# Kernel optimization log

Measured on AMD Instinct MI355X. Metric: run time of the kernel, lower is better.

## Reference

```python
import jax, jax.numpy as jnp
import numpy as np

EPS = 1e-12   # F.normalize eps
COS_EPS = 1e-8  # F.cosine_similarity eps

B, S, V, D, P, L = 4, 2048, 64, 1024, 8, 24
H = D // 24            # prefix_transform bottleneck = 42
K = 2 * L * D          # 49152 output feature dim


def setup_inputs() -> dict:
    key = jax.random.key(0)
    ks = jax.random.split(key, 8)
    return {
        "prefix": jax.random.randint(ks[0], (B, V), 0, V),
        "ctx_embeds": jax.random.normal(ks[1], (B, S, D), jnp.float32),
        "tables": jax.random.normal(ks[2], (P, V, D), jnp.float32) * 0.02,
        "lora_prefix_emb": jax.random.normal(ks[3], (P, D), jnp.float32),
        "w1": jax.random.normal(ks[4], (D, H), jnp.float32) * 0.02,
        "b1": jnp.zeros((H,), jnp.float32),
        "w2": jax.random.normal(ks[5], (H, K), jnp.float32) * 0.02,
        "b2": jnp.zeros((K,), jnp.float32),
    }


def _gates(ctx_embeds, lora_prefix_emb):
    """select_prefix, vectorized over the num_prefix_set loop.

    The original builds sim_i = bmm(norm(emb), norm(e_i.repeat(B,S,1), dim=0).permute)
    of shape [B,S,S]; since the key is repeated, every column of sim is identical,
    so we carry the column vector [P,B,S] and the math is exact.
    """
    b, s, _ = ctx_embeds.shape
    # normalize embedding over feature dim (F.normalize p=2 dim=2)
    emb_n = ctx_embeds / jnp.maximum(
        jnp.linalg.norm(ctx_embeds, axis=2, keepdims=True), EPS)
    # F.normalize over dim=0 of a tensor repeated B times -> sign(x)/sqrt(B)
    u = lora_prefix_emb / jnp.maximum(
        jnp.sqrt(float(b)) * jnp.abs(lora_prefix_emb), EPS)  # [P,D]
    v = jnp.einsum('bsd,pd->pbs', emb_n, u)          # column of sim matrix
    c = jnp.maximum(v, 0.0)                          # clamp(min=0)
    # F.normalize over last dim (length S, all entries equal c) -> c/(sqrt(S)*c)
    n = c / jnp.maximum(jnp.sqrt(float(s)) * c, EPS)
    w = jax.nn.softmax(n, axis=2)                    # softmax over token dim (dim=1 in torch layout)
    a_v = jnp.einsum('pbs,bsd->pbd', w, ctx_embeds)  # attended value per expert
    e_norm = jnp.linalg.norm(lora_prefix_emb, axis=1)          # [P]
    a_norm = jnp.linalg.norm(a_v, axis=2)                      # [P,B]
    cos = jnp.einsum('pd,pbd->pb', lora_prefix_emb, a_v) / \
        jnp.maximum(e_norm[:, None] * a_norm, COS_EPS)
    return jax.nn.softmax(cos.T, axis=-1)            # self.s_t, [B,P]


def reference(prefix, ctx_embeds, tables, lora_prefix_emb, w1, b1, w2, b2):
    s_t = _gates(ctx_embeds, lora_prefix_emb)        # [B,P]
    # forward() re-applies softmax to self.s_t (faithful double softmax)
    gate = jax.nn.softmax(s_t, axis=-1)              # [B,P]
    tok = tables[:, prefix]                          # [P,B,V,D] per-expert embedding lookup
    h = jnp.tanh(jnp.einsum('pbvd,dh->pbvh', tok, w1) + b1)
    pkv = jnp.einsum('pbvh,hk->pbvk', h, w2) + b2    # [P,B,V,K]
    out = jnp.einsum('bp,pbvk->bvk', gate, pkv)      # gated mixture over experts
    return out
```

## Files before the change

kernel.cpp:

```cpp
#include <hip/hip_runtime.h>

#define BB 4
#define SS 2048
#define VV 64
#define DD 1024
#define PP 8
#define HH 42
#define KK 49152

static constexpr float F_EPS = 1e-12f;
static constexpr float ALPHA = 1.02234304f;

__global__ __launch_bounds__(512) void kU_fused(
    const float* __restrict__ ctx, const float* __restrict__ lora,
    const float* __restrict__ tables, const float* __restrict__ w1,
    const float* __restrict__ b1, float* __restrict__ part,
    float* __restrict__ h_all) {
  __shared__ float smem[PP * DD + 16 + 32 * PP];
  const int t = threadIdx.x;
  const int b = blockIdx.y;
  if (blockIdx.x < 64) {
    const int chunk = blockIdx.x;
    float* u_lds = smem;
    float* w_lds = smem + PP * DD + 16;
    for (int i = t; i < PP * DD; i += 512) {
      float e = lora[i];
      u_lds[i] = e / fmaxf(2.0f * fabsf(e), F_EPS);
    }
    __syncthreads();
    const int wave = t >> 6, lane = t & 63;
    const int rbase = b * SS + chunk * 32 + wave * 4;
    const float4* ctx4 = (const float4*)ctx;
    const float4* u4 = (const float4*)u_lds;
    float dot[4][PP];
    #pragma unroll
    for (int i = 0; i < 4; ++i)
      #pragma unroll
      for (int p = 0; p < PP; ++p) dot[i][p] = 0.f;
    #pragma unroll
    for (int j = 0; j < 4; ++j) {
      float4 c[4];
      #pragma unroll
      for (int i = 0; i < 4; ++i)
        c[i] = ctx4[(size_t)(rbase + i) * 256 + j * 64 + lane];
      #pragma unroll
      for (int p = 0; p < PP; ++p) {
        float4 u = u4[p * 256 + j * 64 + lane];
        #pragma unroll
        for (int i = 0; i < 4; ++i)
          dot[i][p] += c[i].x * u.x + c[i].y * u.y + c[i].z * u.z + c[i].w * u.w;
      }
    }
    const int sel = lane & 7;
    #pragma unroll
    for (int i = 0; i < 4; ++i) {
      float d0 = dot[i][0], d1 = dot[i][1], d2 = dot[i][2], d3 = dot[i][3];
      float d4 = dot[i][4], d5 = dot[i][5], d6 = dot[i][6], d7 = dot[i][7];
      #pragma unroll
      for (int m = 1; m <= 4; m <<= 1) {
        d0 += __shfl_xor(d0, m, 64); d1 += __shfl_xor(d1, m, 64);
        d2 += __shfl_xor(d2, m, 64); d3 += __shfl_xor(d3, m, 64);
        d4 += __shfl_xor(d4, m, 64); d5 += __shfl_xor(d5, m, 64);
        d6 += __shfl_xor(d6, m, 64); d7 += __shfl_xor(d7, m, 64);
      }
      float v = d0;
      v = (sel == 1) ? d1 : v; v = (sel == 2) ? d2 : v;
      v = (sel == 3) ? d3 : v; v = (sel == 4) ? d4 : v;
      v = (sel == 5) ? d5 : v; v = (sel == 6) ? d6 : v;
      v = (sel == 7) ? d7 : v;
      v += __shfl_xor(v, 8, 64);
      v += __shfl_xor(v, 16, 64);
      v += __shfl_xor(v, 32, 64);
      if (lane < PP)
        w_lds[(wave * 4 + i) * PP + lane] = (v > 0.0f) ? ALPHA : 1.0f;
    }
    __syncthreads();
    float2 acc[PP];
    #pragma unroll
    for (int p = 0; p < PP; ++p) acc[p] = make_float2(0.f, 0.f);
    const float2* ctx2 = (const float2*)ctx;
    const float4* w4 = (const float4*)w_lds;
    #pragma unroll 4
    for (int sl = 0; sl < 32; ++sl) {
      float2 c = ctx2[(size_t)(b * SS + chunk * 32 + sl) * 512 + t];
      float4 wa = w4[sl * 2];
      float4 wb = w4[sl * 2 + 1];
      float w[PP] = {wa.x, wa.y, wa.z, wa.w, wb.x, wb.y, wb.z, wb.w};
      #pragma unroll
      for (int p = 0; p < PP; ++p) {
        acc[p].x += w[p] * c.x;
        acc[p].y += w[p] * c.y;
      }
    }
    float2* part2 = (float2*)part;
    #pragma unroll
    for (int p = 0; p < PP; ++p)
      part2[(size_t)((b * 64 + chunk) * PP + p) * 512 + t] = acc[p];
  } else {
    float* row_lds = smem;
    float* partial = smem + DD;
    const int r = (blockIdx.x - 64) * 4 + b;
    ((float2*)row_lds)[t] = ((const float2*)(tables + (size_t)r * DD))[t];
    __syncthreads();
    const int h = t & 63, q = t >> 6;
    float acc = 0.0f;
    if (h < HH) {
      const int d0 = q * 128;
      #pragma unroll 8
      for (int dl = 0; dl < 128; ++dl) {
        acc += row_lds[d0 + dl] * w1[(size_t)(d0 + dl) * HH + h];
      }
    }
    partial[q * 64 + h] = acc;
    __syncthreads();
    if (t < HH) {
      float s = 0.0f;
      #pragma unroll
      for (int q8 = 0; q8 < 8; ++q8) s += partial[q8 * 64 + t];
      h_all[(size_t)r * HH + t] = tanhf(s + b1[t]);
    }
  }
}

__global__ __launch_bounds__(256) void k4_cos(
    const float* __restrict__ part, const float* __restrict__ lora,
    float* __restrict__ cos_ws) {
  const int t = threadIdx.x;
  const int p = blockIdx.x, b = blockIdx.y;
  const float4* part4 = (const float4*)part;
  float4 av = make_float4(0.f, 0.f, 0.f, 0.f);
  #pragma unroll 8
  for (int c = 0; c < 64; ++c) {
    float4 x = part4[(size_t)((b * 64 + c) * PP + p) * 256 + t];
    av.x += x.x; av.y += x.y; av.z += x.z; av.w += x.w;
  }
  float4 e = ((const float4*)lora)[p * 256 + t];
  float dt = av.x * e.x + av.y * e.y + av.z * e.z + av.w * e.w;
  float a2 = av.x * av.x + av.y * av.y + av.z * av.z + av.w * av.w;
  float e2 = e.x * e.x + e.y * e.y + e.z * e.z + e.w * e.w;
  #pragma unroll
  for (int m = 32; m >= 1; m >>= 1) {
    dt += __shfl_xor(dt, m, 64);
    a2 += __shfl_xor(a2, m, 64);
    e2 += __shfl_xor(e2, m, 64);
  }
  __shared__ float red[4][3];
  const int wave = t >> 6, lane = t & 63;
  if (lane == 0) { red[wave][0] = dt; red[wave][1] = a2; red[wave][2] = e2; }
  __syncthreads();
  if (t == 0) {
    float Dv = red[0][0] + red[1][0] + red[2][0] + red[3][0];
    float Av = red[0][1] + red[1][1] + red[2][1] + red[3][1];
    float Ev = red[0][2] + red[1][2] + red[2][2] + red[3][2];
    cos_ws[b * PP + p] = Dv / fmaxf(sqrtf(Ev) * sqrtf(Av), 1e-8f);
  }
}

__global__ __launch_bounds__(256) void k7_out(
    const float* __restrict__ w2, const float* __restrict__ b2,
    const float* __restrict__ h_all, const float* __restrict__ cos_ws,
    const int* __restrict__ prefix, float* __restrict__ out) {
  __shared__ float gate_lds[PP];
  __shared__ float hg_lds[HH * 64];
  __shared__ float w2_lds[HH * 128];
  const int t = threadIdx.x;
  const int b = blockIdx.y;
  const size_t kbase = (size_t)blockIdx.x * 128;
  for (int i = t; i < HH * 128; i += 256) {
    int h = i >> 7, kk = i & 127;
    w2_lds[i] = w2[(size_t)h * KK + kbase + kk];
  }
  if (t == 0) {
    float c[PP];
    float m = -1e30f;
    #pragma unroll
    for (int p = 0; p < PP; ++p) { c[p] = cos_ws[b * PP + p]; m = fmaxf(m, c[p]); }
    float s = 0.0f;
    #pragma unroll
    for (int p = 0; p < PP; ++p) { c[p] = expf(c[p] - m); s += c[p]; }
    float inv = 1.0f / s;
    float m2 = -1e30f;
    #pragma unroll
    for (int p = 0; p < PP; ++p) { c[p] *= inv; m2 = fmaxf(m2, c[p]); }
    float s2 = 0.0f;
    #pragma unroll
    for (int p = 0; p < PP; ++p) { c[p] = expf(c[p] - m2); s2 += c[p]; }
    float inv2 = 1.0f / s2;
    #pragma unroll
    for (int p = 0; p < PP; ++p) gate_lds[p] = c[p] * inv2;
  }
  __syncthreads();
  for (int idx = t; idx < 64 * HH; idx += 256) {
    int v = idx / HH;
    int h = idx - v * HH;
    int tokv = prefix[b * VV + v];
    float s = 0.0f;
    #pragma unroll
    for (int p = 0; p < PP; ++p)
      s += gate_lds[p] * h_all[(size_t)(p * VV + tokv) * HH + h];
    hg_lds[h * 64 + v] = s;
  }
  __syncthreads();
  const int tk = t & 31, tb = t >> 5;
  float4 acc[8];
  #pragma unroll
  for (int i = 0; i < 8; ++i) acc[i] = make_float4(0.f, 0.f, 0.f, 0.f);
  const float4* w24 = (const float4*)w2_lds;
  const float4* hg4 = (const float4*)hg_lds;
  #pragma unroll 2
  for (int h = 0; h < HH; ++h) {
    float4 wv = w24[h * 32 + tk];
    float4 g0 = hg4[h * 16 + tb * 2];
    float4 g1 = hg4[h * 16 + tb * 2 + 1];
    float gg[8] = {g0.x, g0.y, g0.z, g0.w, g1.x, g1.y, g1.z, g1.w};
    #pragma unroll
    for (int i = 0; i < 8; ++i) {
      acc[i].x += gg[i] * wv.x;
      acc[i].y += gg[i] * wv.y;
      acc[i].z += gg[i] * wv.z;
      acc[i].w += gg[i] * wv.w;
    }
  }
  float4 b2v = ((const float4*)b2)[(kbase >> 2) + tk];
  float4* out4 = (float4*)out;
  #pragma unroll
  for (int i = 0; i < 8; ++i) {
    int bv = b * 64 + tb * 8 + i;
    float4 o;
    o.x = acc[i].x + b2v.x;
    o.y = acc[i].y + b2v.y;
    o.z = acc[i].z + b2v.z;
    o.w = acc[i].w + b2v.w;
    out4[(((size_t)bv * KK + kbase) >> 2) + tk] = o;
  }
}

extern "C" void kernel_launch(void* const* d_in, const int* in_sizes, int n_in,
                              void* d_out, int out_size, void* d_ws, size_t ws_size,
                              hipStream_t stream) {
  const int* prefix = (const int*)d_in[0];
  const float* ctx = (const float*)d_in[1];
  const float* tables = (const float*)d_in[2];
  const float* lora = (const float*)d_in[3];
  const float* w1 = (const float*)d_in[4];
  const float* b1 = (const float*)d_in[5];
  const float* w2 = (const float*)d_in[6];
  const float* b2 = (const float*)d_in[7];
  float* out = (float*)d_out;
  char* ws = (char*)d_ws;
  float* part = (float*)ws;
  float* cos_ws = (float*)(ws + 8388608);
  float* h_all = (float*)(ws + 8388608 + 128);

  kU_fused<<<dim3(192, 4), 512, 0, stream>>>(ctx, lora, tables, w1, b1, part, h_all);
  k4_cos<<<dim3(8, 4), 256, 0, stream>>>(part, lora, cos_ws);
  k7_out<<<dim3(384, 4), 256, 0, stream>>>(w2, b2, h_all, cos_ws, prefix, out);
}
```

Before: 151.6 us.

## Hoist gate softmax and gated hidden mix out of output kernel into dedicated pass

Splits the cosine reduction into 128 smaller single-wave blocks that emit partial dot and norm sums. A new per-batch kernel computes the double-softmax gate and the gated hidden mix once and writes it to workspace. Previously every one of the 1536 output blocks recomputed that softmax and gathered h_all itself. The output kernel now loads the precomputed mix and writes with nontemporal stores, and the ctx accumulation loop is unrolled further. The cost is one extra kernel launch and a serialized dependency.

```diff
diff --git a/kernel.cpp b/kernel.cpp
--- a/kernel.cpp
+++ b/kernel.cpp
@@ -10,6 +10,8 @@
 
 static constexpr float F_EPS = 1e-12f;
 static constexpr float ALPHA = 1.02234304f;
+
+typedef float f32x4 __attribute__((ext_vector_type(4)));
 
 __global__ __launch_bounds__(512) void kU_fused(
     const float* __restrict__ ctx, const float* __restrict__ lora,
@@ -80,7 +82,7 @@
     for (int p = 0; p < PP; ++p) acc[p] = make_float2(0.f, 0.f);
     const float2* ctx2 = (const float2*)ctx;
     const float4* w4 = (const float4*)w_lds;
-    #pragma unroll 4
+    #pragma unroll 8
     for (int sl = 0; sl < 32; ++sl) {
       float2 c = ctx2[(size_t)(b * SS + chunk * 32 + sl) * 512 + t];
       float4 wa = w4[sl * 2];
@@ -122,19 +124,19 @@
   }
 }
 
-__global__ __launch_bounds__(256) void k4_cos(
+__global__ __launch_bounds__(64) void k4_part(
     const float* __restrict__ part, const float* __restrict__ lora,
-    float* __restrict__ cos_ws) {
-  const int t = threadIdx.x;
-  const int p = blockIdx.x, b = blockIdx.y;
+    float* __restrict__ trip) {
+  const int t = threadIdx.x;
+  const int p = blockIdx.x, b = blockIdx.y, z = blockIdx.z;
   const float4* part4 = (const float4*)part;
   float4 av = make_float4(0.f, 0.f, 0.f, 0.f);
   #pragma unroll 8
   for (int c = 0; c < 64; ++c) {
-    float4 x = part4[(size_t)((b * 64 + c) * PP + p) * 256 + t];
+    float4 x = part4[(size_t)((b * 64 + c) * PP + p) * 256 + z * 64 + t];
     av.x += x.x; av.y += x.y; av.z += x.z; av.w += x.w;
   }
-  float4 e = ((const float4*)lora)[p * 256 + t];
+  float4 e = ((const float4*)lora)[p * 256 + z * 64 + t];
   float dt = av.x * e.x + av.y * e.y + av.z * e.z + av.w * e.w;
   float a2 = av.x * av.x + av.y * av.y + av.z * av.z + av.w * av.w;
   float e2 = e.x * e.x + e.y * e.y + e.z * e.z + e.w * e.w;
@@ -144,23 +146,61 @@
     a2 += __shfl_xor(a2, m, 64);
     e2 += __shfl_xor(e2, m, 64);
   }
-  __shared__ float red[4][3];
-  const int wave = t >> 6, lane = t & 63;
-  if (lane == 0) { red[wave][0] = dt; red[wave][1] = a2; red[wave][2] = e2; }
+  if (t == 0)
+    ((float4*)trip)[(b * PP + p) * 4 + z] = make_float4(dt, a2, e2, 0.f);
+}
+
+__global__ __launch_bounds__(256) void k6_gate_hg(
+    const float* __restrict__ trip, const float* __restrict__ h_all,
+    const int* __restrict__ prefix, float* __restrict__ hg) {
+  __shared__ float gate_lds[PP];
+  const int t = threadIdx.x;
+  const int b = blockIdx.x;
+  if (t < PP) {
+    const float4* tp = (const float4*)trip + ((size_t)b * PP + t) * 4;
+    float dt = 0.f, a2 = 0.f, e2 = 0.f;
+    #pragma unroll
+    for (int z = 0; z < 4; ++z) {
+      float4 x = tp[z];
+      dt += x.x; a2 += x.y; e2 += x.z;
+    }
+    gate_lds[t] = dt / fmaxf(sqrtf(e2) * sqrtf(a2), 1e-8f);
+  }
   __syncthreads();
   if (t == 0) {
-    float Dv = red[0][0] + red[1][0] + red[2][0] + red[3][0];
-    float Av = red[0][1] + red[1][1] + red[2][1] + red[3][1];
-    float Ev = red[0][2] + red[1][2] + red[2][2] + red[3][2];
-    cos_ws[b * PP + p] = Dv / fmaxf(sqrtf(Ev) * sqrtf(Av), 1e-8f);
+    float c[PP];
+    float m = -1e30f;
+    #pragma unroll
+    for (int p = 0; p < PP; ++p) { c[p] = gate_lds[p]; m = fmaxf(m, c[p]); }
+    float s = 0.0f;
+    #pragma unroll
+    for (int p = 0; p < PP; ++p) { c[p] = expf(c[p] - m); s += c[p]; }
+    float inv = 1.0f / s;
+    float m2 = -1e30f;
+    #pragma unroll
+    for (int p = 0; p < PP; ++p) { c[p] *= inv; m2 = fmaxf(m2, c[p]); }
+    float s2 = 0.0f;
+    #pragma unroll
+    for (int p = 0; p < PP; ++p) { c[p] = expf(c[p] - m2); s2 += c[p]; }
+    float inv2 = 1.0f / s2;
+    #pragma unroll
+    for (int p = 0; p < PP; ++p) gate_lds[p] = c[p] * inv2;
+  }
+  __syncthreads();
+  for (int idx = t; idx < VV * HH; idx += 256) {
+    int h = idx >> 6, v = idx & 63;
+    int tokv = prefix[b * VV + v];
+    float s = 0.0f;
+    #pragma unroll
+    for (int p = 0; p < PP; ++p)
+      s += gate_lds[p] * h_all[(size_t)(p * VV + tokv) * HH + h];
+    hg[(size_t)b * (VV * HH) + idx] = s;
   }
 }
 
 __global__ __launch_bounds__(256) void k7_out(
     const float* __restrict__ w2, const float* __restrict__ b2,
-    const float* __restrict__ h_all, const float* __restrict__ cos_ws,
-    const int* __restrict__ prefix, float* __restrict__ out) {
-  __shared__ float gate_lds[PP];
+    const float* __restrict__ hg, float* __restrict__ out) {
   __shared__ float hg_lds[HH * 64];
   __shared__ float w2_lds[HH * 128];
   const int t = threadIdx.x;
@@ -170,35 +210,8 @@
     int h = i >> 7, kk = i & 127;
     w2_lds[i] = w2[(size_t)h * KK + kbase + kk];
   }
-  if (t == 0) {
-    float c[PP];
-    float m = -1e30f;
-    #pragma unroll
-    for (int p = 0; p < PP; ++p) { c[p] = cos_ws[b * PP + p]; m = fmaxf(m, c[p]); }
-    float s = 0.0f;
-    #pragma unroll
-    for (int p = 0; p < PP; ++p) { c[p] = expf(c[p] - m); s += c[p]; }
-    float inv = 1.0f / s;
-    float m2 = -1e30f;
-    #pragma unroll
-    for (int p = 0; p < PP; ++p) { c[p] *= inv; m2 = fmaxf(m2, c[p]); }
-    float s2 = 0.0f;
-    #pragma unroll
-    for (int p = 0; p < PP; ++p) { c[p] = expf(c[p] - m2); s2 += c[p]; }
-    float inv2 = 1.0f / s2;
-    #pragma unroll
-    for (int p = 0; p < PP; ++p) gate_lds[p] = c[p] * inv2;
-  }
-  __syncthreads();
-  for (int idx = t; idx < 64 * HH; idx += 256) {
-    int v = idx / HH;
-    int h = idx - v * HH;
-    int tokv = prefix[b * VV + v];
-    float s = 0.0f;
-    #pragma unroll
-    for (int p = 0; p < PP; ++p)
-      s += gate_lds[p] * h_all[(size_t)(p * VV + tokv) * HH + h];
-    hg_lds[h * 64 + v] = s;
+  for (int i = t; i < HH * 64; i += 256) {
+    hg_lds[i] = hg[(size_t)b * (HH * 64) + i];
   }
   __syncthreads();
   const int tk = t & 31, tb = t >> 5;
@@ -222,16 +235,16 @@
     }
   }
   float4 b2v = ((const float4*)b2)[(kbase >> 2) + tk];
-  float4* out4 = (float4*)out;
+  f32x4* out4 = (f32x4*)out;
   #pragma unroll
   for (int i = 0; i < 8; ++i) {
     int bv = b * 64 + tb * 8 + i;
-    float4 o;
+    f32x4 o;
     o.x = acc[i].x + b2v.x;
     o.y = acc[i].y + b2v.y;
     o.z = acc[i].z + b2v.z;
     o.w = acc[i].w + b2v.w;
-    out4[(((size_t)bv * KK + kbase) >> 2) + tk] = o;
+    __builtin_nontemporal_store(o, out4 + (((size_t)bv * KK + kbase) >> 2) + tk);
   }
 }
 
@@ -249,10 +262,12 @@
   float* out = (float*)d_out;
   char* ws = (char*)d_ws;
   float* part = (float*)ws;
-  float* cos_ws = (float*)(ws + 8388608);
-  float* h_all = (float*)(ws + 8388608 + 128);
+  float* trip = (float*)(ws + 8388608);
+  float* hg = (float*)(ws + 8388608 + 2048);
+  float* h_all = (float*)(ws + 8388608 + 2048 + 43008);
 
   kU_fused<<<dim3(192, 4), 512, 0, stream>>>(ctx, lora, tables, w1, b1, part, h_all);
-  k4_cos<<<dim3(8, 4), 256, 0, stream>>>(part, lora, cos_ws);
-  k7_out<<<dim3(384, 4), 256, 0, stream>>>(w2, b2, h_all, cos_ws, prefix, out);
-}
+  k4_part<<<dim3(8, 4, 4), 64, 0, stream>>>(part, lora, trip);
+  k6_gate_hg<<<dim3(4, 1), 256, 0, stream>>>(trip, h_all, prefix, hg);
+  k7_out<<<dim3(384, 4), 256, 0, stream>>>(w2, b2, hg, out);
+}
```

Result: slower. 160.7 us (+6.1%).

## Fold cosine/gate reduction into first kernel via last-block atomic counter

Applied to the files above, without the earlier changes.

Each gating block now handles 128 rows instead of 32, so there are 16 chunks per batch instead of 64 and fewer partial sums. An atomic counter per batch lets the last finishing chunk block reduce the partials, compute the cosine scores and the double softmax, and write the final gates. This removes the separate k4_cos launch and the per-block softmax in k7_out, at the cost of an extra memset and less parallelism in the gating phase, now 64 blocks instead of 256.

```diff
diff --git a/kernel.cpp b/kernel.cpp
--- a/kernel.cpp
+++ b/kernel.cpp
@@ -7,19 +7,23 @@
 #define PP 8
 #define HH 42
 #define KK 49152
+#define NCHUNK 16
+#define ROWS 128
 
 static constexpr float F_EPS = 1e-12f;
 static constexpr float ALPHA = 1.02234304f;
 
-__global__ __launch_bounds__(512) void kU_fused(
+__global__ __launch_bounds__(512) void kU2(
     const float* __restrict__ ctx, const float* __restrict__ lora,
     const float* __restrict__ tables, const float* __restrict__ w1,
     const float* __restrict__ b1, float* __restrict__ part,
-    float* __restrict__ h_all) {
-  __shared__ float smem[PP * DD + 16 + 32 * PP];
+    float* __restrict__ h_all, float* __restrict__ gate_ws,
+    int* __restrict__ ctr) {
+  __shared__ float smem[PP * DD + 16 + ROWS * PP];
+  __shared__ int flag_s;
   const int t = threadIdx.x;
   const int b = blockIdx.y;
-  if (blockIdx.x < 64) {
+  if (blockIdx.x < NCHUNK) {
     const int chunk = blockIdx.x;
     float* u_lds = smem;
     float* w_lds = smem + PP * DD + 16;
@@ -29,50 +33,53 @@
     }
     __syncthreads();
     const int wave = t >> 6, lane = t & 63;
-    const int rbase = b * SS + chunk * 32 + wave * 4;
     const float4* ctx4 = (const float4*)ctx;
     const float4* u4 = (const float4*)u_lds;
-    float dot[4][PP];
-    #pragma unroll
-    for (int i = 0; i < 4; ++i)
-      #pragma unroll
-      for (int p = 0; p < PP; ++p) dot[i][p] = 0.f;
-    #pragma unroll
-    for (int j = 0; j < 4; ++j) {
-      float4 c[4];
+    const int sel = lane & 7;
+    for (int g = 0; g < 4; ++g) {
+      const int rloc = wave * 16 + g * 4;
+      const int rbase = b * SS + chunk * ROWS + rloc;
+      float dot[4][PP];
       #pragma unroll
       for (int i = 0; i < 4; ++i)
-        c[i] = ctx4[(size_t)(rbase + i) * 256 + j * 64 + lane];
-      #pragma unroll
-      for (int p = 0; p < PP; ++p) {
-        float4 u = u4[p * 256 + j * 64 + lane];
+        #pragma unroll
+        for (int p = 0; p < PP; ++p) dot[i][p] = 0.f;
+      #pragma unroll
+      for (int j = 0; j < 4; ++j) {
+        float4 c[4];
         #pragma unroll
         for (int i = 0; i < 4; ++i)
-          dot[i][p] += c[i].x * u.x + c[i].y * u.y + c[i].z * u.z + c[i].w * u.w;
-      }
-    }
-    const int sel = lane & 7;
-    #pragma unroll
-    for (int i = 0; i < 4; ++i) {
-      float d0 = dot[i][0], d1 = dot[i][1], d2 = dot[i][2], d3 = dot[i][3];
-      float d4 = dot[i][4], d5 = dot[i][5], d6 = dot[i][6], d7 = dot[i][7];
-      #pragma unroll
-      for (int m = 1; m <= 4; m <<= 1) {
-        d0 += __shfl_xor(d0, m, 64); d1 += __shfl_xor(d1, m, 64);
-        d2 += __shfl_xor(d2, m, 64); d3 += __shfl_xor(d3, m, 64);
-        d4 += __shfl_xor(d4, m, 64); d5 += __shfl_xor(d5, m, 64);
-        d6 += __shfl_xor(d6, m, 64); d7 += __shfl_xor(d7, m, 64);
-      }
-      float v = d0;
-      v = (sel == 1) ? d1 : v; v = (sel == 2) ? d2 : v;
-      v = (sel == 3) ? d3 : v; v = (sel == 4) ? d4 : v;
-      v = (sel == 5) ? d5 : v; v = (sel == 6) ? d6 : v;
-      v = (sel == 7) ? d7 : v;
-      v += __shfl_xor(v, 8, 64);
-      v += __shfl_xor(v, 16, 64);
-      v += __shfl_xor(v, 32, 64);
-      if (lane < PP)
-        w_lds[(wave * 4 + i) * PP + lane] = (v > 0.0f) ? ALPHA : 1.0f;
+          c[i] = ctx4[(size_t)(rbase + i) * 256 + j * 64 + lane];
+        #pragma unroll
+        for (int p = 0; p < PP; ++p) {
+          float4 u = u4[p * 256 + j * 64 + lane];
+          #pragma unroll
+          for (int i = 0; i < 4; ++i)
+            dot[i][p] += c[i].x * u.x + c[i].y * u.y + c[i].z * u.z + c[i].w * u.w;
+        }
+      }
+      #pragma unroll
+      for (int i = 0; i < 4; ++i) {
+        float d0 = dot[i][0], d1 = dot[i][1], d2 = dot[i][2], d3 = dot[i][3];
+        float d4 = dot[i][4], d5 = dot[i][5], d6 = dot[i][6], d7 = dot[i][7];
+        #pragma unroll
+        for (int m = 1; m <= 4; m <<= 1) {
+          d0 += __shfl_xor(d0, m, 64); d1 += __shfl_xor(d1, m, 64);
+          d2 += __shfl_xor(d2, m, 64); d3 += __shfl_xor(d3, m, 64);
+          d4 += __shfl_xor(d4, m, 64); d5 += __shfl_xor(d5, m, 64);
+          d6 += __shfl_xor(d6, m, 64); d7 += __shfl_xor(d7, m, 64);
+        }
+        float v = d0;
+        v = (sel == 1) ? d1 : v; v = (sel == 2) ? d2 : v;
+        v = (sel == 3) ? d3 : v; v = (sel == 4) ? d4 : v;
+        v = (sel == 5) ? d5 : v; v = (sel == 6) ? d6 : v;
+        v = (sel == 7) ? d7 : v;
+        v += __shfl_xor(v, 8, 64);
+        v += __shfl_xor(v, 16, 64);
+        v += __shfl_xor(v, 32, 64);
+        if (lane < PP)
+          w_lds[(rloc + i) * PP + lane] = (v > 0.0f) ? ALPHA : 1.0f;
+      }
     }
     __syncthreads();
     float2 acc[PP];
@@ -81,8 +88,8 @@
     const float2* ctx2 = (const float2*)ctx;
     const float4* w4 = (const float4*)w_lds;
     #pragma unroll 4
-    for (int sl = 0; sl < 32; ++sl) {
-      float2 c = ctx2[(size_t)(b * SS + chunk * 32 + sl) * 512 + t];
+    for (int sl = 0; sl < ROWS; ++sl) {
+      float2 c = ctx2[(size_t)(b * SS + chunk * ROWS + sl) * 512 + t];
       float4 wa = w4[sl * 2];
       float4 wb = w4[sl * 2 + 1];
       float w[PP] = {wa.x, wa.y, wa.z, wa.w, wb.x, wb.y, wb.z, wb.w};
@@ -95,11 +102,82 @@
     float2* part2 = (float2*)part;
     #pragma unroll
     for (int p = 0; p < PP; ++p)
-      part2[(size_t)((b * 64 + chunk) * PP + p) * 512 + t] = acc[p];
+      part2[(size_t)((b * NCHUNK + chunk) * PP + p) * 512 + t] = acc[p];
+    if (t == 0) {
+      __threadfence();
+      flag_s = atomicAdd(&ctr[b], 1);
+    }
+    __syncthreads();
+    if (flag_s == NCHUNK - 1) {
+      __threadfence();
+      const float2* p2 = (const float2*)part;
+      float dt[PP], a2[PP], e2[PP];
+      #pragma unroll
+      for (int p = 0; p < PP; ++p) {
+        float avx = 0.f, avy = 0.f;
+        #pragma unroll 4
+        for (int c = 0; c < NCHUNK; ++c) {
+          float2 x = p2[(size_t)((b * NCHUNK + c) * PP + p) * 512 + t];
+          avx += x.x; avy += x.y;
+        }
+        float2 e = ((const float2*)lora)[p * 512 + t];
+        dt[p] = avx * e.x + avy * e.y;
+        a2[p] = avx * avx + avy * avy;
+        e2[p] = e.x * e.x + e.y * e.y;
+      }
+      #pragma unroll
+      for (int p = 0; p < PP; ++p) {
+        #pragma unroll
+        for (int m = 32; m >= 1; m >>= 1) {
+          dt[p] += __shfl_xor(dt[p], m, 64);
+          a2[p] += __shfl_xor(a2[p], m, 64);
+          e2[p] += __shfl_xor(e2[p], m, 64);
+        }
+      }
+      float* red = smem;
+      __syncthreads();
+      if (lane == 0) {
+        #pragma unroll
+        for (int p = 0; p < PP; ++p) {
+          red[(wave * PP + p) * 3 + 0] = dt[p];
+          red[(wave * PP + p) * 3 + 1] = a2[p];
+          red[(wave * PP + p) * 3 + 2] = e2[p];
+        }
+      }
+      __syncthreads();
+      if (t < PP) {
+        float Dv = 0.f, Av = 0.f, Ev = 0.f;
+        #pragma unroll
+        for (int w8 = 0; w8 < 8; ++w8) {
+          Dv += red[(w8 * PP + t) * 3 + 0];
+          Av += red[(w8 * PP + t) * 3 + 1];
+          Ev += red[(w8 * PP + t) * 3 + 2];
+        }
+        red[256 + t] = Dv / fmaxf(sqrtf(Ev) * sqrtf(Av), 1e-8f);
+      }
+      __syncthreads();
+      if (t < PP) {
+        float c[PP];
+        float m = -1e30f;
+        #pragma unroll
+        for (int p = 0; p < PP; ++p) { c[p] = red[256 + p]; m = fmaxf(m, c[p]); }
+        float s = 0.0f;
+        #pragma unroll
+        for (int p = 0; p < PP; ++p) { c[p] = expf(c[p] - m); s += c[p]; }
+        float inv = 1.0f / s;
+        float m2 = -1e30f;
+        #pragma unroll
+        for (int p = 0; p < PP; ++p) { c[p] *= inv; m2 = fmaxf(m2, c[p]); }
+        float s2 = 0.0f;
+        #pragma unroll
+        for (int p = 0; p < PP; ++p) { c[p] = expf(c[p] - m2); s2 += c[p]; }
+        gate_ws[b * PP + t] = c[t] / s2;
+      }
+    }
   } else {
     float* row_lds = smem;
     float* partial = smem + DD;
-    const int r = (blockIdx.x - 64) * 4 + b;
+    const int r = (blockIdx.x - NCHUNK) * 4 + b;
     ((float2*)row_lds)[t] = ((const float2*)(tables + (size_t)r * DD))[t];
     __syncthreads();
     const int h = t & 63, q = t >> 6;
@@ -122,43 +200,9 @@
   }
 }
 
-__global__ __launch_bounds__(256) void k4_cos(
-    const float* __restrict__ part, const float* __restrict__ lora,
-    float* __restrict__ cos_ws) {
-  const int t = threadIdx.x;
-  const int p = blockIdx.x, b = blockIdx.y;
-  const float4* part4 = (const float4*)part;
-  float4 av = make_float4(0.f, 0.f, 0.f, 0.f);
-  #pragma unroll 8
-  for (int c = 0; c < 64; ++c) {
-    float4 x = part4[(size_t)((b * 64 + c) * PP + p) * 256 + t];
-    av.x += x.x; av.y += x.y; av.z += x.z; av.w += x.w;
-  }
-  float4 e = ((const float4*)lora)[p * 256 + t];
-  float dt = av.x * e.x + av.y * e.y + av.z * e.z + av.w * e.w;
-  float a2 = av.x * av.x + av.y * av.y + av.z * av.z + av.w * av.w;
-  float e2 = e.x * e.x + e.y * e.y + e.z * e.z + e.w * e.w;
-  #pragma unroll
-  for (int m = 32; m >= 1; m >>= 1) {
-    dt += __shfl_xor(dt, m, 64);
-    a2 += __shfl_xor(a2, m, 64);
-    e2 += __shfl_xor(e2, m, 64);
-  }
-  __shared__ float red[4][3];
-  const int wave = t >> 6, lane = t & 63;
-  if (lane == 0) { red[wave][0] = dt; red[wave][1] = a2; red[wave][2] = e2; }
-  __syncthreads();
-  if (t == 0) {
-    float Dv = red[0][0] + red[1][0] + red[2][0] + red[3][0];
-    float Av = red[0][1] + red[1][1] + red[2][1] + red[3][1];
-    float Ev = red[0][2] + red[1][2] + red[2][2] + red[3][2];
-    cos_ws[b * PP + p] = Dv / fmaxf(sqrtf(Ev) * sqrtf(Av), 1e-8f);
-  }
-}
-
 __global__ __launch_bounds__(256) void k7_out(
     const float* __restrict__ w2, const float* __restrict__ b2,
-    const float* __restrict__ h_all, const float* __restrict__ cos_ws,
+    const float* __restrict__ h_all, const float* __restrict__ gate_ws,
     const int* __restrict__ prefix, float* __restrict__ out) {
   __shared__ float gate_lds[PP];
   __shared__ float hg_lds[HH * 64];
@@ -170,25 +214,7 @@
     int h = i >> 7, kk = i & 127;
     w2_lds[i] = w2[(size_t)h * KK + kbase + kk];
   }
-  if (t == 0) {
-    float c[PP];
-    float m = -1e30f;
-    #pragma unroll
-    for (int p = 0; p < PP; ++p) { c[p] = cos_ws[b * PP + p]; m = fmaxf(m, c[p]); }
-    float s = 0.0f;
-    #pragma unroll
-    for (int p = 0; p < PP; ++p) { c[p] = expf(c[p] - m); s += c[p]; }
-    float inv = 1.0f / s;
-    float m2 = -1e30f;
-    #pragma unroll
-    for (int p = 0; p < PP; ++p) { c[p] *= inv; m2 = fmaxf(m2, c[p]); }
-    float s2 = 0.0f;
-    #pragma unroll
-    for (int p = 0; p < PP; ++p) { c[p] = expf(c[p] - m2); s2 += c[p]; }
-    float inv2 = 1.0f / s2;
-    #pragma unroll
-    for (int p = 0; p < PP; ++p) gate_lds[p] = c[p] * inv2;
-  }
+  if (t < PP) gate_lds[t] = gate_ws[b * PP + t];
   __syncthreads();
   for (int idx = t; idx < 64 * HH; idx += 256) {
     int v = idx / HH;
@@ -249,10 +275,12 @@
   float* out = (float*)d_out;
   char* ws = (char*)d_ws;
   float* part = (float*)ws;
-  float* cos_ws = (float*)(ws + 8388608);
-  float* h_all = (float*)(ws + 8388608 + 128);
-
-  kU_fused<<<dim3(192, 4), 512, 0, stream>>>(ctx, lora, tables, w1, b1, part, h_all);
-  k4_cos<<<dim3(8, 4), 256, 0, stream>>>(part, lora, cos_ws);
-  k7_out<<<dim3(384, 4), 256, 0, stream>>>(w2, b2, h_all, cos_ws, prefix, out);
+  float* gate_ws = (float*)(ws + 2097152);
+  int* ctr = (int*)(ws + 2097152 + 128);
+  float* h_all = (float*)(ws + 2097152 + 128 + 16);
+
+  hipMemsetAsync(ctr, 0, 4 * sizeof(int), stream);
+  kU2<<<dim3(16 + 128, 4), 512, 0, stream>>>(ctx, lora, tables, w1, b1, part,
+                                             h_all, gate_ws, ctr);
+  k7_out<<<dim3(384, 4), 256, 0, stream>>>(w2, b2, h_all, gate_ws, prefix, out);
 }
```

After: 183.4 us. 1.21x slower.

## Move table-row bottleneck projection from gate kernel into cosine kernel

Applied to the files above, without the earlier changes.

The per-row tables·w1 tanh projection moves out of the first kernel, which now only computes the gate partial sums across 64x4 blocks. It now runs in the same launch as the cosine reduction, 32 cosine blocks plus 512 row blocks of 512 threads each. The aim is to fill the nearly empty cosine launch with independent work and give the gate kernel a homogeneous grid. It also vectorises the u normalisation loads to float4. The cost is that the projection now waits for the gate kernel to finish rather than overlapping with it.

```diff
diff --git a/kernel.cpp b/kernel.cpp
--- a/kernel.cpp
+++ b/kernel.cpp
@@ -7,99 +7,152 @@
 #define PP 8
 #define HH 42
 #define KK 49152
+#define NCHUNK 64
 
 static constexpr float F_EPS = 1e-12f;
 static constexpr float ALPHA = 1.02234304f;
 
-__global__ __launch_bounds__(512) void kU_fused(
+__global__ __launch_bounds__(512) void kU(
     const float* __restrict__ ctx, const float* __restrict__ lora,
-    const float* __restrict__ tables, const float* __restrict__ w1,
-    const float* __restrict__ b1, float* __restrict__ part,
-    float* __restrict__ h_all) {
+    float* __restrict__ part) {
   __shared__ float smem[PP * DD + 16 + 32 * PP];
   const int t = threadIdx.x;
   const int b = blockIdx.y;
-  if (blockIdx.x < 64) {
-    const int chunk = blockIdx.x;
-    float* u_lds = smem;
-    float* w_lds = smem + PP * DD + 16;
-    for (int i = t; i < PP * DD; i += 512) {
-      float e = lora[i];
-      u_lds[i] = e / fmaxf(2.0f * fabsf(e), F_EPS);
-    }
-    __syncthreads();
-    const int wave = t >> 6, lane = t & 63;
-    const int rbase = b * SS + chunk * 32 + wave * 4;
-    const float4* ctx4 = (const float4*)ctx;
-    const float4* u4 = (const float4*)u_lds;
-    float dot[4][PP];
+  const int chunk = blockIdx.x;
+  float* u_lds = smem;
+  float* w_lds = smem + PP * DD + 16;
+  {
+    const float4* lora4 = (const float4*)lora;
+    float4* u4w = (float4*)u_lds;
+    #pragma unroll
+    for (int i = t; i < PP * DD / 4; i += 512) {
+      float4 e = lora4[i];
+      float4 u;
+      u.x = e.x / fmaxf(2.0f * fabsf(e.x), F_EPS);
+      u.y = e.y / fmaxf(2.0f * fabsf(e.y), F_EPS);
+      u.z = e.z / fmaxf(2.0f * fabsf(e.z), F_EPS);
+      u.w = e.w / fmaxf(2.0f * fabsf(e.w), F_EPS);
+      u4w[i] = u;
+    }
+  }
+  __syncthreads();
+  const int wave = t >> 6, lane = t & 63;
+  const int rbase = b * SS + chunk * 32 + wave * 4;
+  const float4* ctx4 = (const float4*)ctx;
+  const float4* u4 = (const float4*)u_lds;
+  float dot[4][PP];
+  #pragma unroll
+  for (int i = 0; i < 4; ++i)
+    #pragma unroll
+    for (int p = 0; p < PP; ++p) dot[i][p] = 0.f;
+  #pragma unroll
+  for (int j = 0; j < 4; ++j) {
+    float4 c[4];
     #pragma unroll
     for (int i = 0; i < 4; ++i)
-      #pragma unroll
-      for (int p = 0; p < PP; ++p) dot[i][p] = 0.f;
-    #pragma unroll
-    for (int j = 0; j < 4; ++j) {
-      float4 c[4];
+      c[i] = ctx4[(size_t)(rbase + i) * 256 + j * 64 + lane];
+    #pragma unroll
+    for (int p = 0; p < PP; ++p) {
+      float4 u = u4[p * 256 + j * 64 + lane];
       #pragma unroll
       for (int i = 0; i < 4; ++i)
-        c[i] = ctx4[(size_t)(rbase + i) * 256 + j * 64 + lane];
+        dot[i][p] += c[i].x * u.x + c[i].y * u.y + c[i].z * u.z + c[i].w * u.w;
+    }
+  }
+  const int sel = lane & 7;
+  #pragma unroll
+  for (int i = 0; i < 4; ++i) {
+    float d0 = dot[i][0], d1 = dot[i][1], d2 = dot[i][2], d3 = dot[i][3];
+    float d4 = dot[i][4], d5 = dot[i][5], d6 = dot[i][6], d7 = dot[i][7];
+    #pragma unroll
+    for (int m = 1; m <= 4; m <<= 1) {
+      d0 += __shfl_xor(d0, m, 64); d1 += __shfl_xor(d1, m, 64);
+      d2 += __shfl_xor(d2, m, 64); d3 += __shfl_xor(d3, m, 64);
+      d4 += __shfl_xor(d4, m, 64); d5 += __shfl_xor(d5, m, 64);
+      d6 += __shfl_xor(d6, m, 64); d7 += __shfl_xor(d7, m, 64);
+    }
+    float v = d0;
+    v = (sel == 1) ? d1 : v; v = (sel == 2) ? d2 : v;
+    v = (sel == 3) ? d3 : v; v = (sel == 4) ? d4 : v;
+    v = (sel == 5) ? d5 : v; v = (sel == 6) ? d6 : v;
+    v = (sel == 7) ? d7 : v;
+    v += __shfl_xor(v, 8, 64);
+    v += __shfl_xor(v, 16, 64);
+    v += __shfl_xor(v, 32, 64);
+    if (lane < PP)
+      w_lds[(wave * 4 + i) * PP + lane] = (v > 0.0f) ? ALPHA : 1.0f;
+  }
+  __syncthreads();
+  float2 acc[PP];
+  #pragma unroll
+  for (int p = 0; p < PP; ++p) acc[p] = make_float2(0.f, 0.f);
+  const float2* ctx2 = (const float2*)ctx;
+  const float4* w4 = (const float4*)w_lds;
+  #pragma unroll 4
+  for (int sl = 0; sl < 32; ++sl) {
+    float2 c = ctx2[(size_t)(b * SS + chunk * 32 + sl) * 512 + t];
+    float4 wa = w4[sl * 2];
+    float4 wb = w4[sl * 2 + 1];
+    float w[PP] = {wa.x, wa.y, wa.z, wa.w, wb.x, wb.y, wb.z, wb.w};
+    #pragma unroll
+    for (int p = 0; p < PP; ++p) {
+      acc[p].x += w[p] * c.x;
+      acc[p].y += w[p] * c.y;
+    }
+  }
+  float2* part2 = (float2*)part;
+  #pragma unroll
+  for (int p = 0; p < PP; ++p)
+    part2[(size_t)((b * NCHUNK + chunk) * PP + p) * 512 + t] = acc[p];
+}
+
+__global__ __launch_bounds__(512) void k4h(
+    const float* __restrict__ part, const float* __restrict__ lora,
+    const float* __restrict__ tables, const float* __restrict__ w1,
+    const float* __restrict__ b1, float* __restrict__ cos_ws,
+    float* __restrict__ h_all) {
+  __shared__ float smem[DD + 512];
+  const int t = threadIdx.x;
+  if (blockIdx.x < 32) {
+    const int p = blockIdx.x & 7, b = blockIdx.x >> 3;
+    const float2* p2 = (const float2*)part;
+    float avx = 0.f, avy = 0.f;
+    #pragma unroll 8
+    for (int c = 0; c < NCHUNK; ++c) {
+      float2 x = p2[(size_t)((b * NCHUNK + c) * PP + p) * 512 + t];
+      avx += x.x; avy += x.y;
+    }
+    float2 e = ((const float2*)lora)[p * 512 + t];
+    float dt = avx * e.x + avy * e.y;
+    float a2 = avx * avx + avy * avy;
+    float e2 = e.x * e.x + e.y * e.y;
+    #pragma unroll
+    for (int m = 32; m >= 1; m >>= 1) {
+      dt += __shfl_xor(dt, m, 64);
+      a2 += __shfl_xor(a2, m, 64);
+      e2 += __shfl_xor(e2, m, 64);
+    }
+    const int wave = t >> 6, lane = t & 63;
+    if (lane == 0) {
+      smem[wave * 3 + 0] = dt;
+      smem[wave * 3 + 1] = a2;
+      smem[wave * 3 + 2] = e2;
+    }
+    __syncthreads();
+    if (t == 0) {
+      float Dv = 0.f, Av = 0.f, Ev = 0.f;
       #pragma unroll
-      for (int p = 0; p < PP; ++p) {
-        float4 u = u4[p * 256 + j * 64 + lane];
-        #pragma unroll
-        for (int i = 0; i < 4; ++i)
-          dot[i][p] += c[i].x * u.x + c[i].y * u.y + c[i].z * u.z + c[i].w * u.w;
+      for (int w8 = 0; w8 < 8; ++w8) {
+        Dv += smem[w8 * 3 + 0];
+        Av += smem[w8 * 3 + 1];
+        Ev += smem[w8 * 3 + 2];
       }
-    }
-    const int sel = lane & 7;
-    #pragma unroll
-    for (int i = 0; i < 4; ++i) {
-      float d0 = dot[i][0], d1 = dot[i][1], d2 = dot[i][2], d3 = dot[i][3];
-      float d4 = dot[i][4], d5 = dot[i][5], d6 = dot[i][6], d7 = dot[i][7];
-      #pragma unroll
-      for (int m = 1; m <= 4; m <<= 1) {
-        d0 += __shfl_xor(d0, m, 64); d1 += __shfl_xor(d1, m, 64);
-        d2 += __shfl_xor(d2, m, 64); d3 += __shfl_xor(d3, m, 64);
-        d4 += __shfl_xor(d4, m, 64); d5 += __shfl_xor(d5, m, 64);
-        d6 += __shfl_xor(d6, m, 64); d7 += __shfl_xor(d7, m, 64);
-      }
-      float v = d0;
-      v = (sel == 1) ? d1 : v; v = (sel == 2) ? d2 : v;
-      v = (sel == 3) ? d3 : v; v = (sel == 4) ? d4 : v;
-      v = (sel == 5) ? d5 : v; v = (sel == 6) ? d6 : v;
-      v = (sel == 7) ? d7 : v;
-      v += __shfl_xor(v, 8, 64);
-      v += __shfl_xor(v, 16, 64);
-      v += __shfl_xor(v, 32, 64);
-      if (lane < PP)
-        w_lds[(wave * 4 + i) * PP + lane] = (v > 0.0f) ? ALPHA : 1.0f;
-    }
-    __syncthreads();
-    float2 acc[PP];
-    #pragma unroll
-    for (int p = 0; p < PP; ++p) acc[p] = make_float2(0.f, 0.f);
-    const float2* ctx2 = (const float2*)ctx;
-    const float4* w4 = (const float4*)w_lds;
-    #pragma unroll 4
-    for (int sl = 0; sl < 32; ++sl) {
-      float2 c = ctx2[(size_t)(b * SS + chunk * 32 + sl) * 512 + t];
-      float4 wa = w4[sl * 2];
-      float4 wb = w4[sl * 2 + 1];
-      float w[PP] = {wa.x, wa.y, wa.z, wa.w, wb.x, wb.y, wb.z, wb.w};
-      #pragma unroll
-      for (int p = 0; p < PP; ++p) {
-        acc[p].x += w[p] * c.x;
-        acc[p].y += w[p] * c.y;
-      }
-    }
-    float2* part2 = (float2*)part;
-    #pragma unroll
-    for (int p = 0; p < PP; ++p)
-      part2[(size_t)((b * 64 + chunk) * PP + p) * 512 + t] = acc[p];
+      cos_ws[b * PP + p] = Dv / fmaxf(sqrtf(Ev) * sqrtf(Av), 1e-8f);
+    }
   } else {
     float* row_lds = smem;
     float* partial = smem + DD;
-    const int r = (blockIdx.x - 64) * 4 + b;
+    const int r = blockIdx.x - 32;
     ((float2*)row_lds)[t] = ((const float2*)(tables + (size_t)r * DD))[t];
     __syncthreads();
     const int h = t & 63, q = t >> 6;
@@ -119,40 +172,6 @@
       for (int q8 = 0; q8 < 8; ++q8) s += partial[q8 * 64 + t];
       h_all[(size_t)r * HH + t] = tanhf(s + b1[t]);
     }
-  }
-}
-
-__global__ __launch_bounds__(256) void k4_cos(
-    const float* __restrict__ part, const float* __restrict__ lora,
-    float* __restrict__ cos_ws) {
-  const int t = threadIdx.x;
-  const int p = blockIdx.x, b = blockIdx.y;
-  const float4* part4 = (const float4*)part;
-  float4 av = make_float4(0.f, 0.f, 0.f, 0.f);
-  #pragma unroll 8
-  for (int c = 0; c < 64; ++c) {
-    float4 x = part4[(size_t)((b * 64 + c) * PP + p) * 256 + t];
-    av.x += x.x; av.y += x.y; av.z += x.z; av.w += x.w;
-  }
-  float4 e = ((const float4*)lora)[p * 256 + t];
-  float dt = av.x * e.x + av.y * e.y + av.z * e.z + av.w * e.w;
-  float a2 = av.x * av.x + av.y * av.y + av.z * av.z + av.w * av.w;
-  float e2 = e.x * e.x + e.y * e.y + e.z * e.z + e.w * e.w;
-  #pragma unroll
-  for (int m = 32; m >= 1; m >>= 1) {
-    dt += __shfl_xor(dt, m, 64);
-    a2 += __shfl_xor(a2, m, 64);
-    e2 += __shfl_xor(e2, m, 64);
-  }
-  __shared__ float red[4][3];
-  const int wave = t >> 6, lane = t & 63;
-  if (lane == 0) { red[wave][0] = dt; red[wave][1] = a2; red[wave][2] = e2; }
-  __syncthreads();
-  if (t == 0) {
-    float Dv = red[0][0] + red[1][0] + red[2][0] + red[3][0];
-    float Av = red[0][1] + red[1][1] + red[2][1] + red[3][1];
-    float Ev = red[0][2] + red[1][2] + red[2][2] + red[3][2];
-    cos_ws[b * PP + p] = Dv / fmaxf(sqrtf(Ev) * sqrtf(Av), 1e-8f);
   }
 }
 
@@ -252,7 +271,8 @@
   float* cos_ws = (float*)(ws + 8388608);
   float* h_all = (float*)(ws + 8388608 + 128);
 
-  kU_fused<<<dim3(192, 4), 512, 0, stream>>>(ctx, lora, tables, w1, b1, part, h_all);
-  k4_cos<<<dim3(8, 4), 256, 0, stream>>>(part, lora, cos_ws);
+  kU<<<dim3(64, 4), 512, 0, stream>>>(ctx, lora, part);
+  k4h<<<dim3(32 + 512), 512, 0, stream>>>(part, lora, tables, w1, b1,
+                                          cos_ws, h_all);
   k7_out<<<dim3(384, 4), 256, 0, stream>>>(w2, b2, h_all, cos_ws, prefix, out);
 }
```

After: 148.1 us. -2.3%, faster.
